# Optimization experiments

Hardware: AMD Instinct MI355X
Metric: run time of the kernel (lower is better)

## Reference

```python
import jax, jax.numpy as jnp
import numpy as np

DIM = 1024
NUM_HEADS = 16
HEAD_DIM = DIM // NUM_HEADS


def setup_inputs() -> dict:
    key = jax.random.key(0)
    ks = jax.random.split(key, 5)
    scale = 1.0 / np.sqrt(DIM)
    return {
        "x": jax.random.normal(ks[0], (2, 2048, DIM), dtype=jnp.float32),
        "qkv_w": jax.random.normal(ks[1], (3 * DIM, DIM), dtype=jnp.float32) * scale,
        "qkv_b": jax.random.normal(ks[2], (3 * DIM,), dtype=jnp.float32) * 0.01,
        "proj_w": jax.random.normal(ks[3], (DIM, DIM), dtype=jnp.float32) * scale,
        "proj_b": jax.random.normal(ks[4], (DIM,), dtype=jnp.float32) * 0.01,
    }


def reference(x, qkv_w, qkv_b, proj_w, proj_b):
    B, N, D = x.shape
    H, Hd = NUM_HEADS, HEAD_DIM
    # fused QKV projection: [B,N,3D]
    qkv = jnp.einsum('bnd,ed->bne', x, qkv_w) + qkv_b
    qkv = qkv.reshape(B, N, 3, H, Hd)
    q = qkv[:, :, 0].transpose(0, 2, 1, 3)  # [B,H,N,Hd]
    k = qkv[:, :, 1].transpose(0, 2, 1, 3)
    v = qkv[:, :, 2].transpose(0, 2, 1, 3)
    scale = 1.0 / jnp.sqrt(jnp.asarray(Hd, dtype=x.dtype))
    scores = jnp.einsum('bhqd,bhkd->bhqk', q, k) * scale  # [B,H,N,N]
    attn = jax.nn.softmax(scores, axis=-1)
    out = jnp.einsum('bhqk,bhkd->bhqd', attn, v)  # [B,H,N,Hd]
    out = out.transpose(0, 2, 1, 3).reshape(B, N, D)
    return jnp.einsum('bnd,ed->bne', out, proj_w) + proj_b
```

## Files before the change

### kernel.cpp

```cpp
#include <hip/hip_runtime.h>
#include <hip/hip_bf16.h>
#include <stdint.h>


typedef __bf16 bf16;
typedef __bf16 bf16x2 __attribute__((ext_vector_type(2)));
typedef __bf16 bf16x4 __attribute__((ext_vector_type(4)));
typedef __bf16 bf16x8 __attribute__((ext_vector_type(8)));
typedef float  f32x4  __attribute__((ext_vector_type(4)));
typedef float  f32x16 __attribute__((ext_vector_type(16)));
typedef uint32_t u32x4 __attribute__((ext_vector_type(4)));

#define QSCALE 0.18033688011112042f

__device__ __forceinline__ void gload_lds16(const void* g, void* l) {
    __builtin_amdgcn_global_load_lds(
        (const __attribute__((address_space(1))) void*)(uintptr_t)g,
        (__attribute__((address_space(3))) void*)(uint32_t)(uintptr_t)l,
        16, 0, 0);
}

__device__ __forceinline__ uint32_t pkbf(float a, float b) {
    bf16x2 t = { (bf16)a, (bf16)b };
    return __builtin_bit_cast(uint32_t, t);
}

__global__ void cast_all(const float* __restrict__ x,
                         const float* __restrict__ qw,
                         const float* __restrict__ pw,
                         bf16* __restrict__ xb, bf16* __restrict__ wq,
                         bf16* __restrict__ wp) {
    const int stride = 2048 * 256;
    for (int i = blockIdx.x * blockDim.x + threadIdx.x; i < 2097152; i += stride) {
        const float4* src; bf16x4* dst; int off;
        if (i < 1048576)      { src = (const float4*)x;  dst = (bf16x4*)xb; off = i; }
        else if (i < 1835008) { src = (const float4*)qw; dst = (bf16x4*)wq; off = i - 1048576; }
        else                  { src = (const float4*)pw; dst = (bf16x4*)wp; off = i - 1835008; }
        float4 v = src[off];
        bf16x4 o = { (bf16)v.x, (bf16)v.y, (bf16)v.z, (bf16)v.w };
        dst[off] = o;
    }
}

template<int EPI>
__global__ __launch_bounds__(256) void gemm128(
    const bf16* __restrict__ A,
    const bf16* __restrict__ Bw,
    const float* __restrict__ bias,
    float* __restrict__ outF,
    bf16* __restrict__ qb, bf16* __restrict__ kf, bf16* __restrict__ vf,
    int K)
{
    __shared__ __align__(16) char gsm[EPI == 0 ? 36864 : 32768];
    bf16* ct = (bf16*)gsm;
    const int tid  = threadIdx.x;
    const int lane = tid & 63, w = tid >> 6;
    const int g = lane >> 4, lr = lane & 15;
    const int wr = w >> 1, wc = w & 1;
    int mt, nt;
    {
        int bid = blockIdx.x;
        int xcd = bid & 7, i = bid >> 3;
        if (EPI == 0) {
            mt = xcd * 4 + i / 24;
            nt = i % 24;
        } else {
            mt = xcd * 4 + i / 8;
            nt = i % 8;
        }
    }
    const int mbase = mt * 128, nbase = nt * 128;

    f32x4 acc[4][4] = {};

    auto stg = [&](int buf, int it) {
        const bf16* Ag = A  + (size_t)mbase * K + it * 32;
        const bf16* Bg = Bw + (size_t)nbase * K + it * 32;
        bf16* as = (bf16*)(gsm + buf * 16384);
        bf16* bs = (bf16*)(gsm + buf * 16384 + 8192);
        int c0 = tid, c1 = 256 + tid;
        gload_lds16(Ag + (size_t)(c0 >> 2) * K + (c0 & 3) * 8, as + c0 * 8);
        gload_lds16(Bg + (size_t)(c0 >> 2) * K + (c0 & 3) * 8, bs + c0 * 8);
        gload_lds16(Ag + (size_t)(c1 >> 2) * K + (c1 & 3) * 8, as + c1 * 8);
        gload_lds16(Bg + (size_t)(c1 >> 2) * K + (c1 & 3) * 8, bs + c1 * 8);
    };

    const int nIt = K >> 5;
    stg(0, 0);
    __syncthreads();

    #pragma unroll 2
    for (int it = 0; it < nIt; ++it) {
        const int cur = it & 1;
        if (it + 1 < nIt) stg(cur ^ 1, it + 1);

        const bf16* as = (const bf16*)(gsm + cur * 16384);
        const bf16* bs = as + 4096;
        bf16x8 af[4], bfr[4];
        #pragma unroll
        for (int mi = 0; mi < 4; ++mi)
            af[mi] = *(const bf16x8*)(as + (wr * 64 + mi * 16 + lr) * 32 + g * 8);
        #pragma unroll
        for (int ni = 0; ni < 4; ++ni)
            bfr[ni] = *(const bf16x8*)(bs + (wc * 64 + ni * 16 + lr) * 32 + g * 8);
        #pragma unroll
        for (int mi = 0; mi < 4; ++mi)
            #pragma unroll
            for (int ni = 0; ni < 4; ++ni)
                acc[mi][ni] = __builtin_amdgcn_mfma_f32_16x16x32_bf16(
                    af[mi], bfr[ni], acc[mi][ni], 0, 0, 0);

        __syncthreads();
    }

    if (EPI == 1) {
        #pragma unroll
        for (int ni = 0; ni < 4; ++ni) {
            int e = nbase + wc * 64 + ni * 16 + lr;
            float bv = bias[e];
            #pragma unroll
            for (int mi = 0; mi < 4; ++mi) {
                #pragma unroll
                for (int r = 0; r < 4; ++r) {
                    int token = mbase + wr * 64 + mi * 16 + g * 4 + r;
                    outF[(size_t)token * 1024 + e] = acc[mi][ni][r] + bv;
                }
            }
        }
    } else {
        const int sec = nbase >> 10;
        #pragma unroll
        for (int ni = 0; ni < 4; ++ni) {
            int ec = wc * 64 + ni * 16 + lr;
            float bv = bias[nbase + ec];
            #pragma unroll
            for (int mi = 0; mi < 4; ++mi) {
                #pragma unroll
                for (int r = 0; r < 4; ++r) {
                    int tl = wr * 64 + mi * 16 + g * 4 + r;
                    float v = acc[mi][ni][r] + bv;
                    if (sec == 0) v *= QSCALE;
                    int row = (sec == 2) ? ec : tl;
                    int col = (sec == 2) ? tl : ec;
                    ct[row * 144 + col] = (bf16)v;
                }
            }
        }
        __syncthreads();
        const int b  = mbase >> 11;
        const int h0 = (nbase & 1023) >> 6;
        const int mb = mbase & 2047;
        #pragma unroll
        for (int si = 0; si < 8; ++si) {
            int c   = si * 256 + tid;
            int hh  = c >> 10;
            int w10 = c & 1023;
            int bh  = b * 16 + h0 + hh;
            int lrow, lcol;
            size_t gaddr;
            bf16* dst;
            if (sec == 0) {
                int nl = w10 >> 3, d0 = (w10 & 7) * 8;
                lrow = nl; lcol = hh * 64 + d0;
                gaddr = ((size_t)bh * 2048 + mb + nl) * 64 + d0;
                dst = qb;
            } else if (sec == 1) {
                int o = w10 * 8;
                int frag = o >> 9, l = (o >> 3) & 63;
                int nl = (frag >> 2) * 32 + (l & 31);
                int d0 = (frag & 3) * 16 + (l >> 5) * 8;
                lrow = nl; lcol = hh * 64 + d0;
                gaddr = ((size_t)(bh * 64 + (mb >> 5))) * 2048 + o;
                dst = kf;
            } else {
                int o = w10 * 8;
                int n6 = o >> 12, r2 = o & 4095;
                int d5 = r2 >> 11, r3 = r2 & 2047;
                int nc = r3 >> 9,  l  = (r3 >> 3) & 63;
                int d  = d5 * 32 + (l & 31);
                int n0 = n6 * 64 + nc * 16 + (l >> 5) * 8;
                lrow = hh * 64 + d; lcol = n0;
                gaddr = ((size_t)(bh * 32 + (mb >> 6))) * 4096 + o;
                dst = vf;
            }
            *(bf16x8*)(dst + gaddr) = *(const bf16x8*)(&ct[lrow * 144 + lcol]);
        }
    }
}

__global__ __launch_bounds__(512, 2) void attn32(
    const bf16* __restrict__ Q,
    const bf16* __restrict__ Kf,
    const bf16* __restrict__ Vf,
    bf16* __restrict__ Ao,
    int Nseq)
{
    __shared__ __align__(16) char smem[65536];
    bf16*  KsB = (bf16*)smem;
    bf16*  VsB = (bf16*)(smem + 32768);
    float* xch = (float*)smem;
    bf16*  otp = (bf16*)(smem + 36864);

    const int tid  = threadIdx.x;
    const int lane = tid & 63;
    const int u    = tid >> 6;
    const int half = u >> 2, qw = u & 3;
    const int hi = lane >> 5, ql = lane & 31;
    const int bid = blockIdx.x;
    const int xcd = bid & 7, ii = bid >> 3;
    const int bh = xcd * 4 + (ii >> 3), qc = ii & 7;
    const int h = bh & 15, b = bh >> 4;
    const int q0 = qc * 256 + qw * 64;

    const bf16* Qh  = Q  + (size_t)bh * Nseq * 64;
    const bf16* Kfh = Kf + (size_t)bh * Nseq * 64;
    const bf16* Vfh = Vf + (size_t)bh * Nseq * 64;

    bf16x8 qfA[4], qfB[4];
    #pragma unroll
    for (int c = 0; c < 4; ++c) {
        qfA[c] = *(const bf16x8*)(Qh + (size_t)(q0 + ql) * 64 + c * 16 + hi * 8);
        qfB[c] = *(const bf16x8*)(Qh + (size_t)(q0 + 32 + ql) * 64 + c * 16 + hi * 8);
    }

    bf16x8 vones;
    #pragma unroll
    for (int i = 0; i < 8; ++i) vones[i] = (bf16)1.0f;

    f32x16 o0A = {}, o1A = {}, laA = {};
    f32x16 o0B = {}, o1B = {}, laB = {};

    const int nch = (Nseq >> 6) >> 1;
    const int hk  = half * nch;

    auto stage = [&](int buf, int t) {
        const bf16* Kc = Kfh + (size_t)(hk + t) * 4096;
        const bf16* Vc = Vfh + (size_t)(hk + t) * 4096;
        bf16* kd = KsB + (half * 2 + buf) * 4096;
        bf16* vd = VsB + (half * 2 + buf) * 4096;
        int ht = tid & 255;
        gload_lds16(Kc + ht * 8,        kd + ht * 8);
        gload_lds16(Kc + 2048 + ht * 8, kd + 2048 + ht * 8);
        gload_lds16(Vc + ht * 8,        vd + ht * 8);
        gload_lds16(Vc + 2048 + ht * 8, vd + 2048 + ht * 8);
    };

    stage(0, 0);
    __syncthreads();

    #pragma unroll 2
    for (int t = 0; t < nch; ++t) {
        const int cur = t & 1;
        if (t + 1 < nch) stage(cur ^ 1, t + 1);

        const bf16* kl = KsB + (half * 2 + cur) * 4096;
        const bf16* vl = VsB + (half * 2 + cur) * 4096;
        bf16x8 kin[8], vfr[8];
        #pragma unroll
        for (int i = 0; i < 8; ++i)
            kin[i] = *(const bf16x8*)(kl + i * 512 + lane * 8);
        #pragma unroll
        for (int i = 0; i < 8; ++i)
            vfr[i] = *(const bf16x8*)(vl + i * 512 + lane * 8);

        {
            f32x16 s0 = {}, s1 = {};
            #pragma unroll
            for (int c = 0; c < 4; ++c) {
                s0 = __builtin_amdgcn_mfma_f32_32x32x16_bf16(kin[c],     qfA[c], s0, 0, 0, 0);
                s1 = __builtin_amdgcn_mfma_f32_32x32x16_bf16(kin[4 + c], qfA[c], s1, 0, 0, 0);
            }
            float p0[16], p1[16];
            #pragma unroll
            for (int r = 0; r < 16; ++r) { p0[r] = __builtin_amdgcn_exp2f(s0[r]); }
            #pragma unroll
            for (int r = 0; r < 16; ++r) { p1[r] = __builtin_amdgcn_exp2f(s1[r]); }
            bf16x8 pfr[4];
            #pragma unroll
            for (int f = 0; f < 4; ++f) {
                const float* pp = (f < 2) ? p0 : p1;
                const int base = (f & 1) * 8;
                union { uint32_t u[4]; bf16x8 v; } pw;
                #pragma unroll
                for (int wd = 0; wd < 2; ++wd) {
                    uint32_t X = pkbf(pp[base + 2*wd], pp[base + 2*wd + 1]);
                    uint32_t Y = pkbf(pp[base + 4 + 2*wd], pp[base + 4 + 2*wd + 1]);
                    auto rr = __builtin_amdgcn_permlane32_swap((int)X, (int)Y, false, false);
                    pw.u[wd]     = (uint32_t)rr[0];
                    pw.u[2 + wd] = (uint32_t)rr[1];
                }
                pfr[f] = pw.v;
            }
            #pragma unroll
            for (int f = 0; f < 4; ++f) {
                o0A = __builtin_amdgcn_mfma_f32_32x32x16_bf16(vfr[f],     pfr[f], o0A, 0, 0, 0);
                o1A = __builtin_amdgcn_mfma_f32_32x32x16_bf16(vfr[4 + f], pfr[f], o1A, 0, 0, 0);
                laA = __builtin_amdgcn_mfma_f32_32x32x16_bf16(vones,      pfr[f], laA, 0, 0, 0);
            }
        }
        {
            f32x16 s0 = {}, s1 = {};
            #pragma unroll
            for (int c = 0; c < 4; ++c) {
                s0 = __builtin_amdgcn_mfma_f32_32x32x16_bf16(kin[c],     qfB[c], s0, 0, 0, 0);
                s1 = __builtin_amdgcn_mfma_f32_32x32x16_bf16(kin[4 + c], qfB[c], s1, 0, 0, 0);
            }
            float p0[16], p1[16];
            #pragma unroll
            for (int r = 0; r < 16; ++r) { p0[r] = __builtin_amdgcn_exp2f(s0[r]); }
            #pragma unroll
            for (int r = 0; r < 16; ++r) { p1[r] = __builtin_amdgcn_exp2f(s1[r]); }
            bf16x8 pfr[4];
            #pragma unroll
            for (int f = 0; f < 4; ++f) {
                const float* pp = (f < 2) ? p0 : p1;
                const int base = (f & 1) * 8;
                union { uint32_t u[4]; bf16x8 v; } pw;
                #pragma unroll
                for (int wd = 0; wd < 2; ++wd) {
                    uint32_t X = pkbf(pp[base + 2*wd], pp[base + 2*wd + 1]);
                    uint32_t Y = pkbf(pp[base + 4 + 2*wd], pp[base + 4 + 2*wd + 1]);
                    auto rr = __builtin_amdgcn_permlane32_swap((int)X, (int)Y, false, false);
                    pw.u[wd]     = (uint32_t)rr[0];
                    pw.u[2 + wd] = (uint32_t)rr[1];
                }
                pfr[f] = pw.v;
            }
            #pragma unroll
            for (int f = 0; f < 4; ++f) {
                o0B = __builtin_amdgcn_mfma_f32_32x32x16_bf16(vfr[f],     pfr[f], o0B, 0, 0, 0);
                o1B = __builtin_amdgcn_mfma_f32_32x32x16_bf16(vfr[4 + f], pfr[f], o1B, 0, 0, 0);
                laB = __builtin_amdgcn_mfma_f32_32x32x16_bf16(vones,      pfr[f], laB, 0, 0, 0);
            }
        }

        __syncthreads();
    }

    auto finish = [&](const f32x16& po0, const f32x16& po1, const f32x16& pla, int qp) {
        float lsum = pla[0];
        __syncthreads();
        if (half == 1) {
            float* xp = xch + ((size_t)(qw * 64 + lane)) * 36;
            *(f32x16*)(xp)      = po0;
            *(f32x16*)(xp + 16) = po1;
            xp[32] = lsum;
        }
        __syncthreads();
        if (half == 0) {
            const float* xp = xch + ((size_t)(qw * 64 + lane)) * 36;
            f32x16 oa = *(const f32x16*)(xp);
            f32x16 ob = *(const f32x16*)(xp + 16);
            f32x16 m0 = po0 + oa;
            f32x16 m1 = po1 + ob;
            float ls = lsum + xp[32];
            float linv = __builtin_amdgcn_rcpf(ls);
            #pragma unroll
            for (int qd = 0; qd < 4; ++qd) {
                int dbase = 8 * qd + 4 * hi;
                bf16* orow = otp + (qw * 32 + ql) * 66;
                *(uint32_t*)(orow + dbase)          = pkbf(m0[4*qd] * linv,   m0[4*qd+1] * linv);
                *(uint32_t*)(orow + dbase + 2)      = pkbf(m0[4*qd+2] * linv, m0[4*qd+3] * linv);
                *(uint32_t*)(orow + 32 + dbase)     = pkbf(m1[4*qd] * linv,   m1[4*qd+1] * linv);
                *(uint32_t*)(orow + 32 + dbase + 2) = pkbf(m1[4*qd+2] * linv, m1[4*qd+3] * linv);
            }
            __asm__ volatile("s_waitcnt lgkmcnt(0)" ::: "memory");
            const int t = lane >> 1, e = lane & 1;
            uint32_t rw[16];
            #pragma unroll
            for (int j = 0; j < 16; ++j)
                rw[j] = *(const uint32_t*)(otp + (qw * 32 + t) * 66 + e * 32 + 2 * j);
            size_t gbase = (size_t)(b * Nseq + q0 + qp + t) * 1024 + h * 64 + e * 32;
            #pragma unroll
            for (int v = 0; v < 4; ++v) {
                u32x4 sv = { rw[4*v], rw[4*v+1], rw[4*v+2], rw[4*v+3] };
                *(u32x4*)(Ao + gbase + v * 8) = sv;
            }
        }
    };
    finish(o0A, o1A, laA, 0);
    finish(o0B, o1B, laB, 32);
}

extern "C" void kernel_launch(void* const* d_in, const int* in_sizes, int n_in,
                              void* d_out, int out_size, void* d_ws, size_t ws_size,
                              hipStream_t stream) {
    const float* x      = (const float*)d_in[0];
    const float* qkv_w  = (const float*)d_in[1];
    const float* qkv_b  = (const float*)d_in[2];
    const float* proj_w = (const float*)d_in[3];
    const float* proj_b = (const float*)d_in[4];
    float* out = (float*)d_out;

    char* ws = (char*)d_ws;
    bf16* xb    = (bf16*)(ws);
    bf16* wqkv  = (bf16*)(ws + ((size_t)8  << 20));
    bf16* wproj = (bf16*)(ws + ((size_t)14 << 20));
    bf16* qb    = (bf16*)(ws + ((size_t)16 << 20));
    bf16* kf    = (bf16*)(ws + ((size_t)24 << 20));
    bf16* vf    = (bf16*)(ws + ((size_t)32 << 20));
    bf16* att   = (bf16*)(ws);

    cast_all<<<dim3(2048), dim3(256), 0, stream>>>(x, qkv_w, proj_w, xb, wqkv, wproj);

    gemm128<0><<<dim3(768), dim3(256), 0, stream>>>(
        xb, wqkv, qkv_b, (float*)nullptr, qb, kf, vf, 1024);

    attn32<<<dim3(256), dim3(512), 0, stream>>>(qb, kf, vf, att, 2048);

    gemm128<1><<<dim3(256), dim3(256), 0, stream>>>(
        att, wproj, proj_b, out, (bf16*)nullptr, (bf16*)nullptr, (bf16*)nullptr, 1024);
}
```

Before: 106.3 us.

## Split attention KV range four ways per block and double the grid

The attention kernel now gives each block 128 queries and splits the KV sequence four ways across wave pairs. Previously each block took 256 queries split across two halves. Each KV stage moves to 32-key chunks, and the grid doubles to 512 blocks, which raises parallelism and occupancy across the CUs. The cost is a larger cross-wave reduction through LDS, with three partial outputs summed by the first group, plus more per-chunk synchronisation and smaller MFMA batches per barrier.

New measurement: 112.1 us. 5.5% more time.

```diff
diff --git a/kernel.cpp b/kernel.cpp
--- a/kernel.cpp
+++ b/kernel.cpp
@@ -61,13 +61,8 @@
     {
         int bid = blockIdx.x;
         int xcd = bid & 7, i = bid >> 3;
-        if (EPI == 0) {
-            mt = xcd * 4 + i / 24;
-            nt = i % 24;
-        } else {
-            mt = xcd * 4 + i / 8;
-            nt = i % 8;
-        }
+        if (EPI == 0) { mt = xcd * 4 + i / 24; nt = i % 24; }
+        else          { mt = xcd * 4 + i / 8;  nt = i % 8;  }
     }
     const int mbase = mt * 128, nbase = nt * 128;
 
@@ -199,18 +194,18 @@
     bf16*  KsB = (bf16*)smem;
     bf16*  VsB = (bf16*)(smem + 32768);
     float* xch = (float*)smem;
-    bf16*  otp = (bf16*)(smem + 36864);
+    bf16*  otp = (bf16*)(smem + 55296);
 
     const int tid  = threadIdx.x;
     const int lane = tid & 63;
     const int u    = tid >> 6;
-    const int half = u >> 2, qw = u & 3;
+    const int qw = u & 1, qt = u >> 1;
     const int hi = lane >> 5, ql = lane & 31;
     const int bid = blockIdx.x;
     const int xcd = bid & 7, ii = bid >> 3;
-    const int bh = xcd * 4 + (ii >> 3), qc = ii & 7;
+    const int bh = xcd * 4 + (ii >> 4), qc = ii & 15;
     const int h = bh & 15, b = bh >> 4;
-    const int q0 = qc * 256 + qw * 64;
+    const int q0 = qc * 128 + qw * 64;
 
     const bf16* Qh  = Q  + (size_t)bh * Nseq * 64;
     const bf16* Kfh = Kf + (size_t)bh * Nseq * 64;
@@ -230,108 +225,96 @@
     f32x16 o0A = {}, o1A = {}, laA = {};
     f32x16 o0B = {}, o1B = {}, laB = {};
 
-    const int nch = (Nseq >> 6) >> 1;
-    const int hk  = half * nch;
-
     auto stage = [&](int buf, int t) {
-        const bf16* Kc = Kfh + (size_t)(hk + t) * 4096;
-        const bf16* Vc = Vfh + (size_t)(hk + t) * 4096;
-        bf16* kd = KsB + (half * 2 + buf) * 4096;
-        bf16* vd = VsB + (half * 2 + buf) * 4096;
-        int ht = tid & 255;
+        int c = qt * 16 + t;
+        const bf16* Kc = Kfh + (size_t)c * 2048;
+        const bf16* Vc = Vfh + (size_t)(c >> 1) * 4096 + (c & 1) * 1024;
+        bf16* kd = KsB + (qt * 2 + buf) * 2048;
+        bf16* vd = VsB + (qt * 2 + buf) * 2048;
+        int ht = tid & 127;
         gload_lds16(Kc + ht * 8,        kd + ht * 8);
-        gload_lds16(Kc + 2048 + ht * 8, kd + 2048 + ht * 8);
+        gload_lds16(Kc + 1024 + ht * 8, kd + 1024 + ht * 8);
         gload_lds16(Vc + ht * 8,        vd + ht * 8);
-        gload_lds16(Vc + 2048 + ht * 8, vd + 2048 + ht * 8);
+        gload_lds16(Vc + 2048 + ht * 8, vd + 1024 + ht * 8);
     };
 
     stage(0, 0);
     __syncthreads();
 
     #pragma unroll 2
-    for (int t = 0; t < nch; ++t) {
+    for (int t = 0; t < 16; ++t) {
         const int cur = t & 1;
-        if (t + 1 < nch) stage(cur ^ 1, t + 1);
-
-        const bf16* kl = KsB + (half * 2 + cur) * 4096;
-        const bf16* vl = VsB + (half * 2 + cur) * 4096;
-        bf16x8 kin[8], vfr[8];
-        #pragma unroll
-        for (int i = 0; i < 8; ++i)
+        if (t + 1 < 16) stage(cur ^ 1, t + 1);
+
+        const bf16* kl = KsB + (qt * 2 + cur) * 2048;
+        const bf16* vl = VsB + (qt * 2 + cur) * 2048;
+        bf16x8 kin[4], vfr[4];
+        #pragma unroll
+        for (int i = 0; i < 4; ++i)
             kin[i] = *(const bf16x8*)(kl + i * 512 + lane * 8);
         #pragma unroll
-        for (int i = 0; i < 8; ++i)
+        for (int i = 0; i < 4; ++i)
             vfr[i] = *(const bf16x8*)(vl + i * 512 + lane * 8);
 
         {
-            f32x16 s0 = {}, s1 = {};
-            #pragma unroll
-            for (int c = 0; c < 4; ++c) {
-                s0 = __builtin_amdgcn_mfma_f32_32x32x16_bf16(kin[c],     qfA[c], s0, 0, 0, 0);
-                s1 = __builtin_amdgcn_mfma_f32_32x32x16_bf16(kin[4 + c], qfA[c], s1, 0, 0, 0);
-            }
-            float p0[16], p1[16];
-            #pragma unroll
-            for (int r = 0; r < 16; ++r) { p0[r] = __builtin_amdgcn_exp2f(s0[r]); }
-            #pragma unroll
-            for (int r = 0; r < 16; ++r) { p1[r] = __builtin_amdgcn_exp2f(s1[r]); }
-            bf16x8 pfr[4];
-            #pragma unroll
-            for (int f = 0; f < 4; ++f) {
-                const float* pp = (f < 2) ? p0 : p1;
-                const int base = (f & 1) * 8;
+            f32x16 s = {};
+            #pragma unroll
+            for (int c = 0; c < 4; ++c)
+                s = __builtin_amdgcn_mfma_f32_32x32x16_bf16(kin[c], qfA[c], s, 0, 0, 0);
+            float p[16];
+            #pragma unroll
+            for (int r = 0; r < 16; ++r) p[r] = __builtin_amdgcn_exp2f(s[r]);
+            bf16x8 pfr[2];
+            #pragma unroll
+            for (int f = 0; f < 2; ++f) {
+                const int base = f * 8;
                 union { uint32_t u[4]; bf16x8 v; } pw;
                 #pragma unroll
                 for (int wd = 0; wd < 2; ++wd) {
-                    uint32_t X = pkbf(pp[base + 2*wd], pp[base + 2*wd + 1]);
-                    uint32_t Y = pkbf(pp[base + 4 + 2*wd], pp[base + 4 + 2*wd + 1]);
+                    uint32_t X = pkbf(p[base + 2*wd], p[base + 2*wd + 1]);
+                    uint32_t Y = pkbf(p[base + 4 + 2*wd], p[base + 4 + 2*wd + 1]);
                     auto rr = __builtin_amdgcn_permlane32_swap((int)X, (int)Y, false, false);
                     pw.u[wd]     = (uint32_t)rr[0];
                     pw.u[2 + wd] = (uint32_t)rr[1];
                 }
                 pfr[f] = pw.v;
             }
-            #pragma unroll
-            for (int f = 0; f < 4; ++f) {
-                o0A = __builtin_amdgcn_mfma_f32_32x32x16_bf16(vfr[f],     pfr[f], o0A, 0, 0, 0);
-                o1A = __builtin_amdgcn_mfma_f32_32x32x16_bf16(vfr[4 + f], pfr[f], o1A, 0, 0, 0);
-                laA = __builtin_amdgcn_mfma_f32_32x32x16_bf16(vones,      pfr[f], laA, 0, 0, 0);
-            }
+            o0A = __builtin_amdgcn_mfma_f32_32x32x16_bf16(vfr[0], pfr[0], o0A, 0, 0, 0);
+            o0A = __builtin_amdgcn_mfma_f32_32x32x16_bf16(vfr[1], pfr[1], o0A, 0, 0, 0);
+            o1A = __builtin_amdgcn_mfma_f32_32x32x16_bf16(vfr[2], pfr[0], o1A, 0, 0, 0);
+            o1A = __builtin_amdgcn_mfma_f32_32x32x16_bf16(vfr[3], pfr[1], o1A, 0, 0, 0);
+            laA = __builtin_amdgcn_mfma_f32_32x32x16_bf16(vones,  pfr[0], laA, 0, 0, 0);
+            laA = __builtin_amdgcn_mfma_f32_32x32x16_bf16(vones,  pfr[1], laA, 0, 0, 0);
         }
         {
-            f32x16 s0 = {}, s1 = {};
-            #pragma unroll
-            for (int c = 0; c < 4; ++c) {
-                s0 = __builtin_amdgcn_mfma_f32_32x32x16_bf16(kin[c],     qfB[c], s0, 0, 0, 0);
-                s1 = __builtin_amdgcn_mfma_f32_32x32x16_bf16(kin[4 + c], qfB[c], s1, 0, 0, 0);
-            }
-            float p0[16], p1[16];
-            #pragma unroll
-            for (int r = 0; r < 16; ++r) { p0[r] = __builtin_amdgcn_exp2f(s0[r]); }
-            #pragma unroll
-            for (int r = 0; r < 16; ++r) { p1[r] = __builtin_amdgcn_exp2f(s1[r]); }
-            bf16x8 pfr[4];
-            #pragma unroll
-            for (int f = 0; f < 4; ++f) {
-                const float* pp = (f < 2) ? p0 : p1;
-                const int base = (f & 1) * 8;
+            f32x16 s = {};
+            #pragma unroll
+            for (int c = 0; c < 4; ++c)
+                s = __builtin_amdgcn_mfma_f32_32x32x16_bf16(kin[c], qfB[c], s, 0, 0, 0);
+            float p[16];
+            #pragma unroll
+            for (int r = 0; r < 16; ++r) p[r] = __builtin_amdgcn_exp2f(s[r]);
+            bf16x8 pfr[2];
+            #pragma unroll
+            for (int f = 0; f < 2; ++f) {
+                const int base = f * 8;
                 union { uint32_t u[4]; bf16x8 v; } pw;
                 #pragma unroll
                 for (int wd = 0; wd < 2; ++wd) {
-                    uint32_t X = pkbf(pp[base + 2*wd], pp[base + 2*wd + 1]);
-                    uint32_t Y = pkbf(pp[base + 4 + 2*wd], pp[base + 4 + 2*wd + 1]);
+                    uint32_t X = pkbf(p[base + 2*wd], p[base + 2*wd + 1]);
+                    uint32_t Y = pkbf(p[base + 4 + 2*wd], p[base + 4 + 2*wd + 1]);
                     auto rr = __builtin_amdgcn_permlane32_swap((int)X, (int)Y, false, false);
                     pw.u[wd]     = (uint32_t)rr[0];
                     pw.u[2 + wd] = (uint32_t)rr[1];
                 }
                 pfr[f] = pw.v;
             }
-            #pragma unroll
-            for (int f = 0; f < 4; ++f) {
-                o0B = __builtin_amdgcn_mfma_f32_32x32x16_bf16(vfr[f],     pfr[f], o0B, 0, 0, 0);
-                o1B = __builtin_amdgcn_mfma_f32_32x32x16_bf16(vfr[4 + f], pfr[f], o1B, 0, 0, 0);
-                laB = __builtin_amdgcn_mfma_f32_32x32x16_bf16(vones,      pfr[f], laB, 0, 0, 0);
-            }
+            o0B = __builtin_amdgcn_mfma_f32_32x32x16_bf16(vfr[0], pfr[0], o0B, 0, 0, 0);
+            o0B = __builtin_amdgcn_mfma_f32_32x32x16_bf16(vfr[1], pfr[1], o0B, 0, 0, 0);
+            o1B = __builtin_amdgcn_mfma_f32_32x32x16_bf16(vfr[2], pfr[0], o1B, 0, 0, 0);
+            o1B = __builtin_amdgcn_mfma_f32_32x32x16_bf16(vfr[3], pfr[1], o1B, 0, 0, 0);
+            laB = __builtin_amdgcn_mfma_f32_32x32x16_bf16(vones,  pfr[0], laB, 0, 0, 0);
+            laB = __builtin_amdgcn_mfma_f32_32x32x16_bf16(vones,  pfr[1], laB, 0, 0, 0);
         }
 
         __syncthreads();
@@ -340,20 +323,23 @@
     auto finish = [&](const f32x16& po0, const f32x16& po1, const f32x16& pla, int qp) {
         float lsum = pla[0];
         __syncthreads();
-        if (half == 1) {
-            float* xp = xch + ((size_t)(qw * 64 + lane)) * 36;
+        if (qt != 0) {
+            float* xp = xch + (size_t)(((qt - 1) * 2 + qw) * 64 + lane) * 36;
             *(f32x16*)(xp)      = po0;
             *(f32x16*)(xp + 16) = po1;
             xp[32] = lsum;
         }
         __syncthreads();
-        if (half == 0) {
-            const float* xp = xch + ((size_t)(qw * 64 + lane)) * 36;
-            f32x16 oa = *(const f32x16*)(xp);
-            f32x16 ob = *(const f32x16*)(xp + 16);
-            f32x16 m0 = po0 + oa;
-            f32x16 m1 = po1 + ob;
-            float ls = lsum + xp[32];
+        if (qt == 0) {
+            f32x16 m0 = po0, m1 = po1;
+            float ls = lsum;
+            #pragma unroll
+            for (int s = 0; s < 3; ++s) {
+                const float* xp = xch + (size_t)((s * 2 + qw) * 64 + lane) * 36;
+                m0 += *(const f32x16*)(xp);
+                m1 += *(const f32x16*)(xp + 16);
+                ls += xp[32];
+            }
             float linv = __builtin_amdgcn_rcpf(ls);
             #pragma unroll
             for (int qd = 0; qd < 4; ++qd) {
@@ -406,7 +392,7 @@
     gemm128<0><<<dim3(768), dim3(256), 0, stream>>>(
         xb, wqkv, qkv_b, (float*)nullptr, qb, kf, vf, 1024);
 
-    attn32<<<dim3(256), dim3(512), 0, stream>>>(qb, kf, vf, att, 2048);
+    attn32<<<dim3(512), dim3(512), 0, stream>>>(qb, kf, vf, att, 2048);
 
     gemm128<1><<<dim3(256), dim3(256), 0, stream>>>(
         att, wproj, proj_b, out, (bf16*)nullptr, (bf16*)nullptr, (bf16*)nullptr, 1024);
```
